# Kernel optimization log

Measured on AMD Instinct MI355X. Metric: run time of the kernel, lower is better.

The kernel has to match this reference:

```python
import jax, jax.numpy as jnp
import numpy as np

K = 5
PAD = 2  # same-size output: pad = dilation*(k-1)/2


def _patches(x, k, pad):
    # x: [B, C, H, W] -> [B, C, k, k, H', W'] (matches torch F.unfold + view layout)
    B, C, H, W = x.shape
    p = jax.lax.conv_general_dilated_patches(
        x, (k, k), (1, 1), [(pad, pad), (pad, pad)])
    return p.reshape(B, C, k, k, p.shape[-2], p.shape[-1])


def setup_inputs() -> dict:
    key = jax.random.key(0)
    k1, k2, k3, k4 = jax.random.split(key, 4)
    B, Cin, Cout, Cg, H, W = 4, 32, 32, 8, 128, 128
    x = jax.random.normal(k1, (B, Cin, H, W), jnp.float32)
    guide = jax.random.normal(k2, (B, Cg, H, W), jnp.float32)
    weight = jax.random.normal(k3, (Cout, Cin, K, K), jnp.float32) * 0.05
    bias = jax.random.normal(k4, (Cout,), jnp.float32) * 0.05
    return {"x": x, "guide": guide, "weight": weight, "bias": bias}


def reference(x, guide, weight, bias):
    k = weight.shape[-1]
    # --- packernel2d (gaussian, smooth_kernel_type='none', channel_wise=False) ---
    gp = _patches(guide, k, PAD)                      # [B, Cg, k, k, H, W]
    center = gp[:, :, k // 2, k // 2][:, :, None, None]  # self-tap feature
    d = gp - center
    kernel = jnp.exp(-0.5 * jnp.sum(d * d, axis=1, keepdims=True))  # [B,1,k,k,H,W]
    # --- pacconv2d native path ---
    cols = _patches(x, k, PAD)                        # [B, Cin, k, k, H, W]
    out = jnp.einsum('bjklmn,ojkl->bomn', cols * kernel, weight)
    return out + bias[None, :, None, None]
```

## Files before the change

### kernel.cpp

```cpp
#include <hip/hip_runtime.h>

#define Bn   4
#define CIN  32
#define COUT 32
#define CG   8
#define Hh   128
#define Ww   128
#define KK   5
#define HW   (Hh * Ww)

#define TW   64
#define TH   4
#define PRW  68
#define PRH  8
#define NSLOT (PRW * PRH)

typedef _Float16 h8  __attribute__((ext_vector_type(8)));
typedef _Float16 h4v __attribute__((ext_vector_type(4)));
typedef float    f4  __attribute__((ext_vector_type(4)));

#define XOFF  0
#define XJG   8704
#define WOFF  34816
#define KOFF  60416
#define SMEMB 73216

#define XT_OFF 0
#define GT_OFF 4194304
#define WT_OFF 5242880
#define WS_NEED (5242880 + 51200)

__global__ void transpose_x(const float* __restrict__ x, _Float16* __restrict__ xt) {
    const int m = blockIdx.x, b = blockIdx.y;
    const int n = threadIdx.x & 127, jh = threadIdx.x >> 7;
    const float* xp = x + ((size_t)(b * CIN + jh * 16)) * HW + m * Ww + n;
    h8 v0, v1;
#pragma unroll
    for (int e = 0; e < 8; ++e) {
        v0[e] = (_Float16)xp[(size_t)e * HW];
        v1[e] = (_Float16)xp[(size_t)(e + 8) * HW];
    }
    h8* dst = (h8*)xt + ((size_t)b * HW + m * Ww + n) * 4 + jh * 2;
    dst[0] = v0; dst[1] = v1;
}

__global__ void transpose_g(const float* __restrict__ g, _Float16* __restrict__ gt) {
    const int m = blockIdx.x * 2 + (threadIdx.x >> 7), b = blockIdx.y;
    const int n = threadIdx.x & 127;
    const float* gp = g + (size_t)b * CG * HW + m * Ww + n;
    h8 v;
#pragma unroll
    for (int e = 0; e < 8; ++e) v[e] = (_Float16)gp[(size_t)e * HW];
    ((h8*)gt)[(size_t)b * HW + m * Ww + n] = v;
}

__global__ void transpose_w(const float* __restrict__ w, _Float16* __restrict__ wt) {
    const int idx = blockIdx.x * 512 + threadIdx.x;
    const int ht = idx >> 9;
    const int half = ht / 25, t = ht - half * 25;
    const int rem = idx & 511;
    const int jg = rem >> 7, o = (rem >> 3) & 15, e = rem & 7;
    wt[idx] = (_Float16)w[(size_t)(half * 16 + o) * (CIN * KK * KK) + (jg * 8 + e) * (KK * KK) + t];
}

__global__ __launch_bounds__(512, 4) void pac_mfma3(
    const _Float16* __restrict__ xt, const _Float16* __restrict__ gt,
    const _Float16* __restrict__ wt, const float* __restrict__ bias,
    float* __restrict__ out)
{
    __shared__ __align__(16) unsigned char smem[SMEMB];

    const int tid  = threadIdx.x;
    const int bx   = blockIdx.x;
    const int half = blockIdx.y;
    const int bz   = blockIdx.z;
    const int tm = (bx >> 1) * TH;
    const int tn = (bx & 1) * TW;

    const int pxbase = bz * HW;
#pragma unroll
    for (int it = 0; it < 5; ++it) {
        const int idx = it * 512 + tid;
        if (idx < 2176) {
            const int slot = idx >> 2, jg = idx & 3;
            const int r = slot / PRW;
            const int c = slot - r * PRW;
            const int gm = tm + r - 2, gn = tn + c - 2;
            h8 v = {};
            if ((unsigned)gm < (unsigned)Hh && (unsigned)gn < (unsigned)Ww)
                v = *(const h8*)(xt + ((size_t)(pxbase + gm * Ww + gn)) * 32 + jg * 8);
            *(h8*)(smem + XOFF + jg * XJG + slot * 16) = v;
        }
    }

    const h8* wth = (const h8*)(wt + half * 12800);
#pragma unroll
    for (int it = 0; it < 4; ++it) {
        const int idx = it * 512 + tid;
        if (idx < 1600)
            *(h8*)(smem + WOFF + idx * 16) = wth[idx];
    }

    {
        const int px = tid & 255, th = tid >> 8;
        const int pr = px >> 6, pc = px & 63;
        const int m = tm + pr, n = tn + pc;
        const h8* gtb = (const h8*)gt + (size_t)bz * HW;
        const h8 g0 = gtb[m * Ww + n];
        float cg[8];
#pragma unroll
        for (int c = 0; c < 8; ++c) cg[c] = (float)g0[c];
        int t = 0;
#pragma unroll
        for (int k = 0; k < KK; ++k) {
#pragma unroll
            for (int l = 0; l < KK; ++l) {
                if ((t < 13) == (th == 0)) {
                    const int gm = m + k - 2, gn = n + l - 2;
                    h8 gv = {};
                    if ((unsigned)gm < (unsigned)Hh && (unsigned)gn < (unsigned)Ww)
                        gv = gtb[gm * Ww + gn];
                    float ss = 0.f;
#pragma unroll
                    for (int i = 0; i < 8; ++i) {
                        const float d = (float)gv[i] - cg[i];
                        ss = fmaf(d, d, ss);
                    }
                    *(_Float16*)(smem + KOFF + t * 512 + px * 2) = (_Float16)__expf(-0.5f * ss);
                }
                ++t;
            }
        }
    }

    __syncthreads();

    const int lane = tid & 63;
    const int l15 = lane & 15, kg = lane >> 4;
    const int wv = tid >> 6;
    const int st0 = wv * 32, st1 = st0 + 16;
    const int r0 = wv >> 1;
    const int c00 = (wv & 1) * 32;

    f4 acc0 = {0.f, 0.f, 0.f, 0.f}, acc1 = {0.f, 0.f, 0.f, 0.f};
    const unsigned char* xg = smem + XOFF + kg * XJG;
    const float bv = bias[half * 16 + l15];

    int t = 0;
#pragma unroll
    for (int k = 0; k < KK; ++k) {
#pragma unroll
        for (int l = 0; l < KK; ++l) {
            const int abase = ((r0 + k) * PRW + c00 + l + l15) * 16;
            h8 A0 = *(const h8*)(xg + abase);
            h8 A1 = *(const h8*)(xg + abase + 256);
            h8 Bv = *(const h8*)(smem + WOFF + t * 1024 + kg * 256 + l15 * 16);

            f4 p0 = __builtin_amdgcn_mfma_f32_16x16x32_f16(A0, Bv, (f4){0.f,0.f,0.f,0.f}, 0, 0, 0);
            f4 p1 = __builtin_amdgcn_mfma_f32_16x16x32_f16(A1, Bv, (f4){0.f,0.f,0.f,0.f}, 0, 0, 0);

            h4v k0 = *(const h4v*)(smem + KOFF + t * 512 + (st0 + kg * 4) * 2);
            h4v k1 = *(const h4v*)(smem + KOFF + t * 512 + (st1 + kg * 4) * 2);
#pragma unroll
            for (int i = 0; i < 4; ++i) {
                acc0[i] = fmaf((float)k0[i], p0[i], acc0[i]);
                acc1[i] = fmaf((float)k1[i], p1[i], acc1[i]);
            }
            ++t;
        }
    }

#pragma unroll
    for (int i = 0; i < 4; ++i) { acc0[i] += bv; acc1[i] += bv; }

    __syncthreads();
    float* outst = (float*)smem;
    *(f4*)(outst + l15 * 260 + st0 + kg * 4) = acc0;
    *(f4*)(outst + l15 * 260 + st1 + kg * 4) = acc1;
    __syncthreads();

    const int o = tid >> 5;
    const int p = (tid & 31) * 8;
    f4 v0 = *(const f4*)(outst + o * 260 + p);
    f4 v1 = *(const f4*)(outst + o * 260 + p + 4);
    const int mr = p >> 6, nc = p & 63;
    float* op = out + ((size_t)(bz * COUT + half * 16 + o)) * HW + (size_t)(tm + mr) * Ww + tn + nc;
    *(f4*)op = v0;
    *(f4*)(op + 4) = v1;
}

__global__ __launch_bounds__(512, 4) void pac_mfma2(
    const float* __restrict__ x, const float* __restrict__ guide,
    const float* __restrict__ weight, const float* __restrict__ bias,
    float* __restrict__ out)
{
    __shared__ __align__(16) unsigned char smem[SMEMB];
    const int tid  = threadIdx.x;
    const int bx   = blockIdx.x;
    const int half = blockIdx.y;
    const int bz   = blockIdx.z;
    const int tm = (bx >> 1) * TH;
    const int tn = (bx & 1) * TW;

    const float* xb = x + (size_t)bz * CIN * HW;
#pragma unroll
    for (int it = 0; it < 34; ++it) {
        const int idx  = it * 512 + tid;
        const int j    = idx / NSLOT;
        const int slot = idx - j * NSLOT;
        const int r    = slot / PRW;
        const int c    = slot - r * PRW;
        const int gm = tm + r - 2, gn = tn + c - 2;
        float v = 0.f;
        if ((unsigned)gm < (unsigned)Hh && (unsigned)gn < (unsigned)Ww)
            v = xb[(size_t)j * HW + gm * Ww + gn];
        *(_Float16*)(smem + XOFF + (j >> 3) * XJG + slot * 16 + (j & 7) * 2) = (_Float16)v;
    }
#pragma unroll
    for (int it = 0; it < 25; ++it) {
        const int idx = it * 512 + tid;
        const int o = idx & 15;
        const int j = (idx >> 4) & 31;
        const int t = idx >> 9;
        const float v = weight[(size_t)(half * 16 + o) * (CIN * KK * KK) + j * (KK * KK) + t];
        *(_Float16*)(smem + WOFF + t * 1024 + (j >> 3) * 256 + o * 16 + (j & 7) * 2) = (_Float16)v;
    }
    {
        const int px = tid & 255, th = tid >> 8;
        const int pr = px >> 6, pc = px & 63;
        const int m = tm + pr, n = tn + pc;
        const float* gb = guide + ((size_t)bz * CG) * HW + m * Ww + n;
        float center[CG];
#pragma unroll
        for (int c = 0; c < CG; ++c) center[c] = gb[c * HW];
        int t = 0;
#pragma unroll
        for (int k = 0; k < KK; ++k) {
            const int dm = k - 2;
            const bool rowok = ((unsigned)(m + dm) < (unsigned)Hh);
#pragma unroll
            for (int l = 0; l < KK; ++l) {
                if ((t < 13) == (th == 0)) {
                    const int dn = l - 2;
                    const bool ok = rowok && ((unsigned)(n + dn) < (unsigned)Ww);
                    float ss = 0.f;
#pragma unroll
                    for (int c = 0; c < CG; ++c) {
                        float gv = ok ? gb[c * HW + dm * Ww + dn] : 0.f;
                        float d = gv - center[c];
                        ss = fmaf(d, d, ss);
                    }
                    *(_Float16*)(smem + KOFF + t * 512 + px * 2) = (_Float16)__expf(-0.5f * ss);
                }
                ++t;
            }
        }
    }
    __syncthreads();
    const int lane = tid & 63;
    const int l15 = lane & 15, kg = lane >> 4;
    const int wv = tid >> 6;
    const int st0 = wv * 32, st1 = st0 + 16;
    const int r0 = wv >> 1;
    const int c00 = (wv & 1) * 32;
    f4 acc0 = {0.f, 0.f, 0.f, 0.f}, acc1 = {0.f, 0.f, 0.f, 0.f};
    const unsigned char* xg = smem + XOFF + kg * XJG;
    const float bv = bias[half * 16 + l15];
    int t = 0;
#pragma unroll
    for (int k = 0; k < KK; ++k) {
#pragma unroll
        for (int l = 0; l < KK; ++l) {
            const int abase = ((r0 + k) * PRW + c00 + l + l15) * 16;
            h8 A0 = *(const h8*)(xg + abase);
            h8 A1 = *(const h8*)(xg + abase + 256);
            h8 Bv = *(const h8*)(smem + WOFF + t * 1024 + kg * 256 + l15 * 16);
            f4 p0 = __builtin_amdgcn_mfma_f32_16x16x32_f16(A0, Bv, (f4){0.f,0.f,0.f,0.f}, 0, 0, 0);
            f4 p1 = __builtin_amdgcn_mfma_f32_16x16x32_f16(A1, Bv, (f4){0.f,0.f,0.f,0.f}, 0, 0, 0);
            h4v k0 = *(const h4v*)(smem + KOFF + t * 512 + (st0 + kg * 4) * 2);
            h4v k1 = *(const h4v*)(smem + KOFF + t * 512 + (st1 + kg * 4) * 2);
#pragma unroll
            for (int i = 0; i < 4; ++i) {
                acc0[i] = fmaf((float)k0[i], p0[i], acc0[i]);
                acc1[i] = fmaf((float)k1[i], p1[i], acc1[i]);
            }
            ++t;
        }
    }
#pragma unroll
    for (int i = 0; i < 4; ++i) { acc0[i] += bv; acc1[i] += bv; }
    __syncthreads();
    float* outst = (float*)smem;
    *(f4*)(outst + l15 * 260 + st0 + kg * 4) = acc0;
    *(f4*)(outst + l15 * 260 + st1 + kg * 4) = acc1;
    __syncthreads();
    const int o = tid >> 5;
    const int p = (tid & 31) * 8;
    f4 v0 = *(const f4*)(outst + o * 260 + p);
    f4 v1 = *(const f4*)(outst + o * 260 + p + 4);
    const int mr = p >> 6, nc = p & 63;
    float* op = out + ((size_t)(bz * COUT + half * 16 + o)) * HW + (size_t)(tm + mr) * Ww + tn + nc;
    *(f4*)op = v0;
    *(f4*)(op + 4) = v1;
}

extern "C" void kernel_launch(void* const* d_in, const int* in_sizes, int n_in,
                              void* d_out, int out_size, void* d_ws, size_t ws_size,
                              hipStream_t stream) {
    const float* x      = (const float*)d_in[0];
    const float* guide  = (const float*)d_in[1];
    const float* weight = (const float*)d_in[2];
    const float* bias   = (const float*)d_in[3];
    float* out = (float*)d_out;

    if (ws_size >= (size_t)WS_NEED) {
        _Float16* xt = (_Float16*)((char*)d_ws + XT_OFF);
        _Float16* gt = (_Float16*)((char*)d_ws + GT_OFF);
        _Float16* wt = (_Float16*)((char*)d_ws + WT_OFF);
        transpose_x<<<dim3(Hh, Bn), 256, 0, stream>>>(x, xt);
        transpose_g<<<dim3(Hh / 2, Bn), 256, 0, stream>>>(guide, gt);
        transpose_w<<<dim3(50), 512, 0, stream>>>(weight, wt);
        pac_mfma3<<<dim3(64, 2, Bn), 512, 0, stream>>>(xt, gt, wt, bias, out);
    } else {
        pac_mfma2<<<dim3(64, 2, Bn), 512, 0, stream>>>(x, guide, weight, bias, out);
    }
}
```

Baseline: 27.89 us.

## Merge prep kernels and precompute guide kernel weights once per tile

Replaces the three transpose kernels with one prep launch that also computes the Gaussian adaptive kernel weights per tile into workspace, using an LDS-staged guide halo. The main MFMA kernel now just loads the precomputed fp16 kernel weights instead of recomputing them, and it does so in both output-channel halves. This removes duplicated exp and guide work and two launches. The cost is an extra global round trip for the kernel weights, about 3.2 MB written and read back.

```diff
diff --git a/kernel.cpp b/kernel.cpp
--- a/kernel.cpp
+++ b/kernel.cpp
@@ -26,46 +26,86 @@
 #define SMEMB 73216
 
 #define XT_OFF 0
-#define GT_OFF 4194304
-#define WT_OFF 5242880
-#define WS_NEED (5242880 + 51200)
-
-__global__ void transpose_x(const float* __restrict__ x, _Float16* __restrict__ xt) {
-    const int m = blockIdx.x, b = blockIdx.y;
-    const int n = threadIdx.x & 127, jh = threadIdx.x >> 7;
-    const float* xp = x + ((size_t)(b * CIN + jh * 16)) * HW + m * Ww + n;
-    h8 v0, v1;
-#pragma unroll
-    for (int e = 0; e < 8; ++e) {
-        v0[e] = (_Float16)xp[(size_t)e * HW];
-        v1[e] = (_Float16)xp[(size_t)(e + 8) * HW];
-    }
-    h8* dst = (h8*)xt + ((size_t)b * HW + m * Ww + n) * 4 + jh * 2;
-    dst[0] = v0; dst[1] = v1;
+#define WT_OFF 4194304
+#define KW_OFF 4245504
+#define WS_NEED 7522304
+
+__global__ __launch_bounds__(512) void prep(
+    const float* __restrict__ x, const float* __restrict__ guide,
+    const float* __restrict__ w,
+    _Float16* __restrict__ xt, _Float16* __restrict__ wt, _Float16* __restrict__ kw)
+{
+    const int bid = blockIdx.x;
+    const int tid = threadIdx.x;
+
+    if (bid < 512) {
+        const int b = bid >> 7, m = bid & 127;
+        const int n = tid & 127, jh = tid >> 7;
+        const float* xp = x + ((size_t)(b * CIN + jh * 8)) * HW + m * Ww + n;
+        h8 v;
+#pragma unroll
+        for (int e = 0; e < 8; ++e) v[e] = (_Float16)xp[(size_t)e * HW];
+        ((h8*)xt)[((size_t)b * HW + m * Ww + n) * 4 + jh] = v;
+    } else if (bid < 562) {
+        const int idx = (bid - 512) * 512 + tid;
+        const int ht = idx >> 9;
+        const int half = ht / 25, t = ht - half * 25;
+        const int rem = idx & 511;
+        const int jg = rem >> 7, o = (rem >> 3) & 15, e = rem & 7;
+        wt[idx] = (_Float16)w[(size_t)(half * 16 + o) * (CIN * KK * KK) + (jg * 8 + e) * (KK * KK) + t];
+    } else {
+        __shared__ __align__(16) _Float16 gl[NSLOT * 8];
+        const int tb = bid - 562;
+        const int tile = tb & 63, b = tb >> 6;
+        const int tm = (tile >> 1) * TH, tn = (tile & 1) * TW;
+        const float* gb = guide + (size_t)b * CG * HW;
+#pragma unroll
+        for (int it = 0; it < 2; ++it) {
+            const int slot = it * 512 + tid;
+            if (slot < NSLOT) {
+                const int r = slot / PRW, c = slot - r * PRW;
+                const int gm = tm + r - 2, gn = tn + c - 2;
+                h8 v = {};
+                if ((unsigned)gm < (unsigned)Hh && (unsigned)gn < (unsigned)Ww) {
+#pragma unroll
+                    for (int cg = 0; cg < 8; ++cg)
+                        v[cg] = (_Float16)gb[(size_t)cg * HW + gm * Ww + gn];
+                }
+                *(h8*)(gl + slot * 8) = v;
+            }
+        }
+        __syncthreads();
+        const int px = tid & 255, th = tid >> 8;
+        const int pr = px >> 6, pc = px & 63;
+        const h8 c8 = *(const h8*)(gl + ((pr + 2) * PRW + pc + 2) * 8);
+        float cg[8];
+#pragma unroll
+        for (int i = 0; i < 8; ++i) cg[i] = (float)c8[i];
+        _Float16* kout = kw + ((size_t)(b * 64 + tile) * 25) * 256;
+        int t = 0;
+#pragma unroll
+        for (int k = 0; k < KK; ++k) {
+#pragma unroll
+            for (int l = 0; l < KK; ++l) {
+                if ((t < 13) == (th == 0)) {
+                    const h8 gv = *(const h8*)(gl + ((pr + k) * PRW + pc + l) * 8);
+                    float ss = 0.f;
+#pragma unroll
+                    for (int i = 0; i < 8; ++i) {
+                        const float d = (float)gv[i] - cg[i];
+                        ss = fmaf(d, d, ss);
+                    }
+                    kout[t * 256 + px] = (_Float16)__expf(-0.5f * ss);
+                }
+                ++t;
+            }
+        }
+    }
 }
 
-__global__ void transpose_g(const float* __restrict__ g, _Float16* __restrict__ gt) {
-    const int m = blockIdx.x * 2 + (threadIdx.x >> 7), b = blockIdx.y;
-    const int n = threadIdx.x & 127;
-    const float* gp = g + (size_t)b * CG * HW + m * Ww + n;
-    h8 v;
-#pragma unroll
-    for (int e = 0; e < 8; ++e) v[e] = (_Float16)gp[(size_t)e * HW];
-    ((h8*)gt)[(size_t)b * HW + m * Ww + n] = v;
-}
-
-__global__ void transpose_w(const float* __restrict__ w, _Float16* __restrict__ wt) {
-    const int idx = blockIdx.x * 512 + threadIdx.x;
-    const int ht = idx >> 9;
-    const int half = ht / 25, t = ht - half * 25;
-    const int rem = idx & 511;
-    const int jg = rem >> 7, o = (rem >> 3) & 15, e = rem & 7;
-    wt[idx] = (_Float16)w[(size_t)(half * 16 + o) * (CIN * KK * KK) + (jg * 8 + e) * (KK * KK) + t];
-}
-
-__global__ __launch_bounds__(512, 4) void pac_mfma3(
-    const _Float16* __restrict__ xt, const _Float16* __restrict__ gt,
-    const _Float16* __restrict__ wt, const float* __restrict__ bias,
+__global__ __launch_bounds__(512, 4) void pac_mfma4(
+    const _Float16* __restrict__ xt, const _Float16* __restrict__ wt,
+    const _Float16* __restrict__ kw, const float* __restrict__ bias,
     float* __restrict__ out)
 {
     __shared__ __align__(16) unsigned char smem[SMEMB];
@@ -101,36 +141,12 @@
             *(h8*)(smem + WOFF + idx * 16) = wth[idx];
     }
 
-    {
-        const int px = tid & 255, th = tid >> 8;
-        const int pr = px >> 6, pc = px & 63;
-        const int m = tm + pr, n = tn + pc;
-        const h8* gtb = (const h8*)gt + (size_t)bz * HW;
-        const h8 g0 = gtb[m * Ww + n];
-        float cg[8];
-#pragma unroll
-        for (int c = 0; c < 8; ++c) cg[c] = (float)g0[c];
-        int t = 0;
-#pragma unroll
-        for (int k = 0; k < KK; ++k) {
-#pragma unroll
-            for (int l = 0; l < KK; ++l) {
-                if ((t < 13) == (th == 0)) {
-                    const int gm = m + k - 2, gn = n + l - 2;
-                    h8 gv = {};
-                    if ((unsigned)gm < (unsigned)Hh && (unsigned)gn < (unsigned)Ww)
-                        gv = gtb[gm * Ww + gn];
-                    float ss = 0.f;
-#pragma unroll
-                    for (int i = 0; i < 8; ++i) {
-                        const float d = (float)gv[i] - cg[i];
-                        ss = fmaf(d, d, ss);
-                    }
-                    *(_Float16*)(smem + KOFF + t * 512 + px * 2) = (_Float16)__expf(-0.5f * ss);
-                }
-                ++t;
-            }
-        }
+    const h8* ksrc = (const h8*)(kw + ((size_t)(bz * 64 + bx) * 25) * 256);
+#pragma unroll
+    for (int it = 0; it < 2; ++it) {
+        const int idx = it * 512 + tid;
+        if (idx < 800)
+            *(h8*)(smem + KOFF + idx * 16) = ksrc[idx];
     }
 
     __syncthreads();
@@ -315,12 +331,10 @@
 
     if (ws_size >= (size_t)WS_NEED) {
         _Float16* xt = (_Float16*)((char*)d_ws + XT_OFF);
-        _Float16* gt = (_Float16*)((char*)d_ws + GT_OFF);
         _Float16* wt = (_Float16*)((char*)d_ws + WT_OFF);
-        transpose_x<<<dim3(Hh, Bn), 256, 0, stream>>>(x, xt);
-        transpose_g<<<dim3(Hh / 2, Bn), 256, 0, stream>>>(guide, gt);
-        transpose_w<<<dim3(50), 512, 0, stream>>>(weight, wt);
-        pac_mfma3<<<dim3(64, 2, Bn), 512, 0, stream>>>(xt, gt, wt, bias, out);
+        _Float16* kw = (_Float16*)((char*)d_ws + KW_OFF);
+        prep<<<dim3(818), 512, 0, stream>>>(x, guide, weight, xt, wt, kw);
+        pac_mfma4<<<dim3(64, 2, Bn), 512, 0, stream>>>(xt, wt, kw, bias, out);
     } else {
         pac_mfma2<<<dim3(64, 2, Bn), 512, 0, stream>>>(x, guide, weight, bias, out);
     }
```

Measured after the change: 24.76 us. -11.2%, faster.
